# Optimization experiments

Measured on AMD Instinct MI355X. Metric: run time of the kernel, lower is better.

Reference implementation:

```python
import jax, jax.numpy as jnp
import numpy as np

C = 1024
H = 16
EPS = 1e-5

def layernorm(x, g, b):
    mu = jnp.mean(x, axis=-1, keepdims=True)
    var = jnp.var(x, axis=-1, keepdims=True)
    return (x - mu) * jax.lax.rsqrt(var + EPS) * g + b

def setup_inputs() -> dict:
    key = jax.random.key(0)
    ks = jax.random.split(key, 12)
    s = lambda fan: 1.0 / np.sqrt(fan)
    return {
        "x": jax.random.normal(ks[0], (2, 2048, C), jnp.float32),
        "W_qkv": jax.random.uniform(ks[1], (C, 3 * C), jnp.float32, -s(C), s(C)),
        "W_o": jax.random.uniform(ks[2], (C, C), jnp.float32, -s(C), s(C)),
        "b_o": jnp.zeros((C,), jnp.float32),
        "g1": jnp.ones((C,), jnp.float32),
        "beta1": jnp.zeros((C,), jnp.float32),
        "g2": jnp.ones((C,), jnp.float32),
        "beta2": jnp.zeros((C,), jnp.float32),
        "W_ff1": jax.random.uniform(ks[3], (C, 4 * C), jnp.float32, -s(C), s(C)),
        "b_ff1": jnp.zeros((4 * C,), jnp.float32),
        "W_ff2": jax.random.uniform(ks[4], (4 * C, C), jnp.float32, -s(4 * C), s(4 * C)),
        "b_ff2": jnp.zeros((C,), jnp.float32),
    }

def reference(x, W_qkv, W_o, b_o, g1, beta1, g2, beta2, W_ff1, b_ff1, W_ff2, b_ff2):
    B, T, _ = x.shape
    hd = C // H  # head dim
    # --- self-attention on norm1(x) ---
    h = layernorm(x, g1, beta1)
    qkv = h @ W_qkv                      # [B,T,3C]
    q, k, v = jnp.split(qkv, 3, axis=-1)
    reshp = lambda t: t.reshape(B, T, H, hd).transpose(0, 2, 1, 3)  # [B,H,T,hd]
    q, k, v = reshp(q), reshp(k), reshp(v)
    att = jnp.einsum("bhqd,bhkd->bhqk", q, k) * (hd ** -0.5)
    causal = jnp.tril(jnp.ones((T, T), bool))
    att = jnp.where(causal, att, -jnp.inf)
    att = jax.nn.softmax(att, axis=-1)
    out = jnp.einsum("bhqk,bhkd->bhqd", att, v)
    out = out.transpose(0, 2, 1, 3).reshape(B, T, C)
    x = x + out @ W_o + b_o
    # --- feed-forward on norm2(x) ---
    h = layernorm(x, g2, beta2)
    h = jax.nn.relu(h @ W_ff1 + b_ff1) @ W_ff2 + b_ff2
    return x + h
```

## Files before the change

### kernel.cpp

```cpp
#include <hip/hip_runtime.h>
#include <hip/hip_bf16.h>
#include <stdint.h>


typedef __attribute__((ext_vector_type(8))) short bf16x8;
typedef __attribute__((ext_vector_type(4))) float f32x4;

#define MFMA16(a, b, c) __builtin_amdgcn_mfma_f32_16x16x32_bf16((a), (b), (c), 0, 0, 0)

__device__ __forceinline__ void gload16(const void* g, void* l) {
    __builtin_amdgcn_global_load_lds(
        (const __attribute__((address_space(1))) char*)g,
        (__attribute__((address_space(3))) char*)l, 16, 0, 0);
}

__device__ __forceinline__ int xcd_swizzle(int flat, int nblk) {
    if ((nblk & 7) == 0) {
        const int per = nblk >> 3;
        flat = (flat & 7) * per + (flat >> 3);
    }
    return flat;
}

__global__ __launch_bounds__(256) void tconv_all(
    const float* __restrict__ w0, __hip_bfloat16* __restrict__ o0,
    const float* __restrict__ w1, __hip_bfloat16* __restrict__ o1,
    const float* __restrict__ w2, __hip_bfloat16* __restrict__ o2,
    const float* __restrict__ w3, __hip_bfloat16* __restrict__ o3) {
    __shared__ float tile[64][33];
    const int f = blockIdx.x;
    const float* in; __hip_bfloat16* out; int K, N, nx, t;
    if (f < 1536)      { in = w0; out = o0; K = 1024; N = 3072; nx = 96;  t = f; }
    else if (f < 2048) { in = w1; out = o1; K = 1024; N = 1024; nx = 32;  t = f - 1536; }
    else if (f < 4096) { in = w2; out = o2; K = 1024; N = 4096; nx = 128; t = f - 2048; }
    else               { in = w3; out = o3; K = 4096; N = 1024; nx = 32;  t = f - 4096; }
    const int n0 = (t % nx) * 32, k0 = (t / nx) * 64;
    const int tx = threadIdx.x, ty = threadIdx.y;
#pragma unroll
    for (int i = 0; i < 8; i++)
        tile[i * 8 + ty][tx] = in[(size_t)(k0 + i * 8 + ty) * N + n0 + tx];
    __syncthreads();
    for (int i = ty; i < 32; i += 8) {
        const unsigned short lo =
            __bfloat16_as_ushort(__float2bfloat16(tile[2 * tx][i]));
        const unsigned short hi =
            __bfloat16_as_ushort(__float2bfloat16(tile[2 * tx + 1][i]));
        *(uint32_t*)(out + (size_t)(n0 + i) * K + k0 + 2 * tx) =
            ((uint32_t)hi << 16) | lo;
    }
}

__global__ __launch_bounds__(256) void ln_k(const float* __restrict__ x,
                                            const float* __restrict__ g,
                                            const float* __restrict__ beta,
                                            __hip_bfloat16* __restrict__ out) {
    const int row = blockIdx.x;
    const int tid = threadIdx.x;
    float4 v = ((const float4*)(x + (size_t)row * 1024))[tid];
    float s  = v.x + v.y + v.z + v.w;
    float s2 = v.x * v.x + v.y * v.y + v.z * v.z + v.w * v.w;
    for (int off = 1; off < 64; off <<= 1) {
        s  += __shfl_xor(s,  off, 64);
        s2 += __shfl_xor(s2, off, 64);
    }
    __shared__ float ss[4], ss2[4];
    const int w = tid >> 6, lane = tid & 63;
    if (lane == 0) { ss[w] = s; ss2[w] = s2; }
    __syncthreads();
    s  = ss[0] + ss[1] + ss[2] + ss[3];
    s2 = ss2[0] + ss2[1] + ss2[2] + ss2[3];
    const float mu  = s * (1.0f / 1024.0f);
    const float var = s2 * (1.0f / 1024.0f) - mu * mu;
    const float rs  = rsqrtf(var + 1e-5f);
    float4 gv = ((const float4*)g)[tid];
    float4 bv = ((const float4*)beta)[tid];
    __hip_bfloat16* o = out + (size_t)row * 1024 + tid * 4;
    o[0] = __float2bfloat16((v.x - mu) * rs * gv.x + bv.x);
    o[1] = __float2bfloat16((v.y - mu) * rs * gv.y + bv.y);
    o[2] = __float2bfloat16((v.z - mu) * rs * gv.z + bv.z);
    o[3] = __float2bfloat16((v.w - mu) * rs * gv.w + bv.w);
}

template <int BIAS, int RELU>
__global__ __launch_bounds__(512, 2) void gemm256_k(const __hip_bfloat16* __restrict__ A,
                                                    const __hip_bfloat16* __restrict__ Bt,
                                                    const float* __restrict__ bias,
                                                    __hip_bfloat16* __restrict__ out,
                                                    int M, int N, int K) {
    __align__(16) __shared__ __hip_bfloat16 As[2][2][128 * 64];
    __align__(16) __shared__ __hip_bfloat16 Bs[2][2][128 * 64];

    const int tid  = threadIdx.x;
    const int lane = tid & 63, w = tid >> 6;
    const int wm = w >> 2, wn = w & 3;
    const int nbx = gridDim.x;
    const int flat = xcd_swizzle(blockIdx.y * nbx + blockIdx.x, nbx * gridDim.y);
    const int m0 = (flat / nbx) * 256, n0 = (flat % nbx) * 256;
    const int l16 = lane & 15, quad = lane >> 4;

    const int srw = lane >> 3;
    const int scn = ((lane & 7) - srw) & 7;

    const __hip_bfloat16* gA[2][2];
    const __hip_bfloat16* gB[2][2];
#pragma unroll
    for (int h = 0; h < 2; h++)
#pragma unroll
        for (int i = 0; i < 2; i++) {
            const int r = h * 128 + i * 64 + w * 8 + srw;
            gA[h][i] = A  + (size_t)(m0 + r) * K + scn * 8;
            gB[h][i] = Bt + (size_t)(n0 + r) * K + scn * 8;
        }

    int offA[2][4], offB[2][2];
#pragma unroll
    for (int s = 0; s < 2; s++) {
#pragma unroll
        for (int t = 0; t < 4; t++) {
            const int r = t * 16 + l16;
            offA[s][t] = (r * 8 + ((s * 4 + quad + (r & 7)) & 7)) * 16;
        }
#pragma unroll
        for (int t = 0; t < 2; t++) {
            const int r = (wn & 1) * 64 + t * 16 + l16;
            offB[s][t] = (r * 8 + ((s * 4 + quad + (r & 7)) & 7)) * 16;
        }
    }
    const char* AsW = (const char*)&As[0][wm][0];
    const char* BsW = (const char*)&Bs[0][wn >> 1][0];

    f32x4 acc[8][4] = {};
    bf16x8 a[2][4], b[2][2];

    const int NT = K >> 6;

#define STG_A(ST, SH, D)                                                      \
    do { if ((ST) < NT) {                                                     \
        _Pragma("unroll") for (int i = 0; i < 2; i++)                         \
            gload16(gA[SH][i] + (size_t)(ST) * 64,                            \
                    &As[D][SH][(i * 64 + w * 8) * 64]);                       \
    } } while (0)
#define STG_B(ST, SH, D)                                                      \
    do { if ((ST) < NT) {                                                     \
        _Pragma("unroll") for (int i = 0; i < 2; i++)                         \
            gload16(gB[SH][i] + (size_t)(ST) * 64,                            \
                    &Bs[D][SH][(i * 64 + w * 8) * 64]);                       \
    } } while (0)
#define VM_NONE do {} while (0)
#define VM_P(X)                                                               \
    do { if ((X) < NT) asm volatile("s_waitcnt vmcnt(2)" ::: "memory");       \
         else          asm volatile("s_waitcnt vmcnt(0)" ::: "memory");       \
    } while (0)

#define PH(RDA, MH, RDB, NH, D, STG, VM)                                      \
    do {                                                                      \
        if (RDA) {                                                            \
            _Pragma("unroll") for (int s = 0; s < 2; s++)                     \
            _Pragma("unroll") for (int t = 0; t < 4; t++)                     \
                a[s][t] = *(const bf16x8*)(AsW + (D) * 32768 + (MH) * 8192 +  \
                                           offA[s][t]);                       \
        }                                                                     \
        if (RDB) {                                                            \
            _Pragma("unroll") for (int s = 0; s < 2; s++)                     \
            _Pragma("unroll") for (int t = 0; t < 2; t++)                     \
                b[s][t] = *(const bf16x8*)(BsW + (D) * 32768 + (NH) * 4096 +  \
                                           offB[s][t]);                       \
        }                                                                     \
        STG;                                                                  \
        __builtin_amdgcn_s_barrier();                                         \
        asm volatile("" ::: "memory");                                        \
        __builtin_amdgcn_s_setprio(1);                                        \
        _Pragma("unroll") for (int s = 0; s < 2; s++)                         \
        _Pragma("unroll") for (int ti = 0; ti < 4; ti++)                      \
        _Pragma("unroll") for (int tj = 0; tj < 2; tj++)                      \
            acc[(MH) * 4 + ti][(NH) * 2 + tj] =                               \
                MFMA16(a[s][ti], b[s][tj], acc[(MH) * 4 + ti][(NH) * 2 + tj]);\
        __builtin_amdgcn_s_setprio(0);                                        \
        VM;                                                                   \
        __builtin_amdgcn_s_barrier();                                         \
        asm volatile("" ::: "memory");                                        \
    } while (0)

    STG_A(0, 0, 0); STG_A(0, 1, 0); STG_B(0, 0, 0); STG_B(0, 1, 0);
    STG_A(1, 0, 1);
    asm volatile("s_waitcnt vmcnt(2)" ::: "memory");
    __builtin_amdgcn_s_barrier();
    asm volatile("" ::: "memory");

    for (int T = 0; T < NT; T += 2) {
        PH(1, 0, 1, 0, 0, STG_A(T + 1, 1, 1), VM_NONE);
        PH(0, 0, 1, 1, 0, STG_B(T + 1, 0, 1), VM_NONE);
        PH(1, 1, 0, 1, 0, STG_B(T + 1, 1, 1), VM_NONE);
        PH(0, 1, 1, 0, 0, STG_A(T + 2, 0, 0), VM_P(T + 2));
        PH(1, 0, 1, 0, 1, STG_A(T + 2, 1, 0), VM_NONE);
        PH(0, 0, 1, 1, 1, STG_B(T + 2, 0, 0), VM_NONE);
        PH(1, 1, 0, 1, 1, STG_B(T + 2, 1, 0), VM_NONE);
        PH(0, 1, 1, 0, 1, STG_A(T + 3, 0, 1), VM_P(T + 3));
    }
#undef PH
#undef VM_P
#undef VM_NONE
#undef STG_B
#undef STG_A

#pragma unroll
    for (int mt = 0; mt < 8; mt++)
#pragma unroll
        for (int nt = 0; nt < 4; nt++) {
            const int row = m0 + wm * 128 + mt * 16 + quad * 4;
            const int col = n0 + wn * 64 + nt * 16 + l16;
            const float bv = BIAS ? bias[col] : 0.0f;
#pragma unroll
            for (int r = 0; r < 4; r++) {
                float v = acc[mt][nt][r] + bv;
                if (RELU) v = v > 0.0f ? v : 0.0f;
                out[(size_t)(row + r) * N + col] = __float2bfloat16(v);
            }
        }
}

template <int BIAS, int RELU, int RESID, int OUTBF>
__global__ __launch_bounds__(256, 4) void gemm6464_k(const __hip_bfloat16* __restrict__ A,
                                                     const __hip_bfloat16* __restrict__ Bt,
                                                     const float* __restrict__ bias,
                                                     const float* __restrict__ resid,
                                                     void* __restrict__ out,
                                                     int M, int N, int K) {
    __align__(16) __shared__ __hip_bfloat16 As[2][64 * 64];
    __align__(16) __shared__ __hip_bfloat16 Bs[2][64 * 64];

    const int tid  = threadIdx.x;
    const int lane = tid & 63, w = tid >> 6;
    const int wm = w >> 1, wn = w & 1;
    const int nbx = gridDim.x;
    const int flat = xcd_swizzle(blockIdx.y * nbx + blockIdx.x, nbx * gridDim.y);
    const int m0 = (flat / nbx) * 64, n0 = (flat % nbx) * 64;
    const int l16 = lane & 15, quad = lane >> 4;

    const int srw = lane >> 3;
    const int scn = ((lane & 7) - srw) & 7;

    const __hip_bfloat16* ga[2];
    const __hip_bfloat16* gb[2];
#pragma unroll
    for (int i = 0; i < 2; i++) {
        const int row = i * 32 + w * 8 + srw;
        ga[i] = A  + (size_t)(m0 + row) * K + scn * 8;
        gb[i] = Bt + (size_t)(n0 + row) * K + scn * 8;
    }

    int offA[2][2], offB[2][2];
#pragma unroll
    for (int s = 0; s < 2; s++)
#pragma unroll
        for (int t = 0; t < 2; t++) {
            const int rA = wm * 32 + t * 16 + l16;
            offA[s][t] = (rA * 8 + ((s * 4 + quad + (rA & 7)) & 7)) * 16;
            const int rB = wn * 32 + t * 16 + l16;
            offB[s][t] = (rB * 8 + ((s * 4 + quad + (rB & 7)) & 7)) * 16;
        }

    f32x4 acc[2][2] = {};

#pragma unroll
    for (int i = 0; i < 2; i++) {
        gload16(ga[i], As[0] + (i * 256 + w * 64) * 8);
        gload16(gb[i], Bs[0] + (i * 256 + w * 64) * 8);
        ga[i] += 64; gb[i] += 64;
    }

    const int niter = K >> 6;
    for (int it = 0; it < niter; it++) {
        const int buf = it & 1;
        __syncthreads();
        if (it + 1 < niter) {
#pragma unroll
            for (int i = 0; i < 2; i++) {
                gload16(ga[i], As[buf ^ 1] + (i * 256 + w * 64) * 8);
                gload16(gb[i], Bs[buf ^ 1] + (i * 256 + w * 64) * 8);
                ga[i] += 64; gb[i] += 64;
            }
        }

#pragma unroll
        for (int s = 0; s < 2; s++) {
            bf16x8 af[2], bfr[2];
#pragma unroll
            for (int t = 0; t < 2; t++) {
                af[t]  = *(const bf16x8*)((const char*)As[buf] + offA[s][t]);
                bfr[t] = *(const bf16x8*)((const char*)Bs[buf] + offB[s][t]);
            }
#pragma unroll
            for (int mt = 0; mt < 2; mt++)
#pragma unroll
                for (int nt = 0; nt < 2; nt++)
                    acc[mt][nt] = MFMA16(af[mt], bfr[nt], acc[mt][nt]);
        }
    }

#pragma unroll
    for (int mt = 0; mt < 2; mt++)
#pragma unroll
        for (int nt = 0; nt < 2; nt++) {
            const int row = m0 + wm * 32 + mt * 16 + quad * 4;
            const int col = n0 + wn * 32 + nt * 16 + l16;
            const float bv = BIAS ? bias[col] : 0.0f;
#pragma unroll
            for (int r = 0; r < 4; r++) {
                float v = acc[mt][nt][r] + bv;
                if (RELU) v = v > 0.0f ? v : 0.0f;
                const size_t idx = (size_t)(row + r) * N + col;
                if (RESID) v += resid[idx];
                if (OUTBF) ((__hip_bfloat16*)out)[idx] = __float2bfloat16(v);
                else       ((float*)out)[idx] = v;
            }
        }
}

__global__ __launch_bounds__(256) void vtrans_k(const __hip_bfloat16* __restrict__ qkv,
                                                __hip_bfloat16* __restrict__ vt) {
    const int T = 2048, C3 = 3072;
    const int bh = blockIdx.y, b = bh >> 4, h = bh & 15;
    const int t0 = blockIdx.x * 64;
    const int tx = threadIdx.x, ty = threadIdx.y;
    __shared__ __hip_bfloat16 tile[64][65];
#pragma unroll
    for (int j = 0; j < 16; j++) {
        const int tl = ty * 16 + j;
        tile[tl][tx] = qkv[(size_t)(b * T + t0 + tl) * C3 + 2048 + h * 64 + tx];
    }
    __syncthreads();
#pragma unroll
    for (int j = 0; j < 16; j++) {
        const int d = ty * 16 + j;
        vt[((size_t)bh * 64 + d) * 2048 + t0 + tx] = tile[tx][d];
    }
}

__global__ __launch_bounds__(256, 3) void attn_k(const __hip_bfloat16* __restrict__ qkv,
                                                 const __hip_bfloat16* __restrict__ vt,
                                                 __hip_bfloat16* __restrict__ outp) {
    const int T = 2048, C3 = 3072;
    const int bh = blockIdx.x, b = bh >> 4, h = bh & 15;
    const int qt = 31 - blockIdx.y;
    const int q0 = qt * 64;
    const int tid = threadIdx.x, lane = tid & 63, w = tid >> 6;
    const int l16 = lane & 15, quad = lane >> 4;

    __align__(16) __shared__ __hip_bfloat16 Ks[2][64 * 64];
    __align__(16) __shared__ __hip_bfloat16 Vs[2][64 * 64];
    __align__(16) __shared__ __hip_bfloat16 Pw[4][16 * 72];

    const float sc = 0.125f * 1.44269504f;
    bf16x8 qf0, qf1;
    {
        const __hip_bfloat16* qp =
            qkv + (size_t)(b * T + q0 + w * 16 + l16) * C3 + h * 64;
        bf16x8 a = *(const bf16x8*)(qp + quad * 8);
        bf16x8 c = *(const bf16x8*)(qp + 32 + quad * 8);
#pragma unroll
        for (int i = 0; i < 8; i++) {
            union { unsigned int u; float f; } ua, uc;
            ua.u = ((unsigned int)(unsigned short)a[i]) << 16;
            uc.u = ((unsigned int)(unsigned short)c[i]) << 16;
            qf0[i] = (short)(__bfloat16_as_ushort(__float2bfloat16(ua.f * sc)));
            qf1[i] = (short)(__bfloat16_as_ushort(__float2bfloat16(uc.f * sc)));
        }
    }

    const int srw = lane >> 3;
    const int scn = ((lane & 7) - srw) & 7;
    const __hip_bfloat16* kp[2];
    const __hip_bfloat16* vp[2];
#pragma unroll
    for (int i = 0; i < 2; i++) {
        const int row = i * 32 + w * 8 + srw;
        kp[i] = qkv + (size_t)(b * T + row) * C3 + 1024 + h * 64 + scn * 8;
        vp[i] = vt + ((size_t)bh * 64 + row) * 2048 + scn * 8;
    }

    int offK[2][4];
#pragma unroll
    for (int s = 0; s < 2; s++)
#pragma unroll
        for (int t = 0; t < 4; t++) {
            const int rr = t * 16 + l16;
            offK[s][t] = (rr * 8 + ((s * 4 + quad + (rr & 7)) & 7)) * 16;
        }

    f32x4 oacc[4] = {};
    float lpart[4] = {0.0f, 0.0f, 0.0f, 0.0f};

#pragma unroll
    for (int i = 0; i < 2; i++) {
        gload16(kp[i], Ks[0] + (i * 256 + w * 64) * 8);
        gload16(vp[i], Vs[0] + (i * 256 + w * 64) * 8);
    }

    for (int kt = 0; kt <= qt; kt++) {
        const int buf = kt & 1;
        __syncthreads();
        if (kt < qt) {
#pragma unroll
            for (int i = 0; i < 2; i++) {
                gload16(kp[i] + (size_t)(kt + 1) * 64 * C3,
                        Ks[buf ^ 1] + (i * 256 + w * 64) * 8);
                gload16(vp[i] + (kt + 1) * 64,
                        Vs[buf ^ 1] + (i * 256 + w * 64) * 8);
            }
        }

        f32x4 s4[4];
#pragma unroll
        for (int nt = 0; nt < 4; nt++) {
            bf16x8 kf0 = *(const bf16x8*)((const char*)Ks[buf] + offK[0][nt]);
            bf16x8 kf1 = *(const bf16x8*)((const char*)Ks[buf] + offK[1][nt]);
            f32x4 z = {};
            z = MFMA16(qf0, kf0, z);
            z = MFMA16(qf1, kf1, z);
            s4[nt] = z;
        }

        const bool diag = (kt == qt);
        const int myrow = w * 16 + quad * 4;
#pragma unroll
        for (int nt = 0; nt < 4; nt++) {
            const int col = nt * 16 + l16;
#pragma unroll
            for (int r = 0; r < 4; r++) {
                float p = exp2f(s4[nt][r]);
                if (diag && col > myrow + r) p = 0.0f;
                lpart[r] += p;
                Pw[w][(quad * 4 + r) * 72 + col] = __float2bfloat16(p);
            }
        }

        asm volatile("s_waitcnt lgkmcnt(0)" ::: "memory");

        bf16x8 pf0 = *(const bf16x8*)(&Pw[w][l16 * 72 + quad * 8]);
        bf16x8 pf1 = *(const bf16x8*)(&Pw[w][l16 * 72 + 32 + quad * 8]);
#pragma unroll
        for (int dt = 0; dt < 4; dt++) {
            bf16x8 vf0 = *(const bf16x8*)((const char*)Vs[buf] + offK[0][dt]);
            bf16x8 vf1 = *(const bf16x8*)((const char*)Vs[buf] + offK[1][dt]);
            oacc[dt] = MFMA16(pf0, vf0, oacc[dt]);
            oacc[dt] = MFMA16(pf1, vf1, oacc[dt]);
        }
    }

#pragma unroll
    for (int off = 1; off < 16; off <<= 1)
#pragma unroll
        for (int r = 0; r < 4; r++)
            lpart[r] += __shfl_xor(lpart[r], off, 64);

    float rl[4];
#pragma unroll
    for (int r = 0; r < 4; r++) rl[r] = 1.0f / lpart[r];
#pragma unroll
    for (int dt = 0; dt < 4; dt++)
#pragma unroll
        for (int r = 0; r < 4; r++) {
            const int row = q0 + w * 16 + quad * 4 + r;
            outp[(size_t)(b * T + row) * 1024 + h * 64 + dt * 16 + l16] =
                __float2bfloat16(oacc[dt][r] * rl[r]);
        }
}

extern "C" void kernel_launch(void* const* d_in, const int* in_sizes, int n_in,
                              void* d_out, int out_size, void* d_ws, size_t ws_size,
                              hipStream_t stream) {
    const float* x     = (const float*)d_in[0];
    const float* Wqkv  = (const float*)d_in[1];
    const float* Wo    = (const float*)d_in[2];
    const float* b_o   = (const float*)d_in[3];
    const float* g1    = (const float*)d_in[4];
    const float* beta1 = (const float*)d_in[5];
    const float* g2    = (const float*)d_in[6];
    const float* beta2 = (const float*)d_in[7];
    const float* Wff1  = (const float*)d_in[8];
    const float* bff1  = (const float*)d_in[9];
    const float* Wff2  = (const float*)d_in[10];
    const float* bff2  = (const float*)d_in[11];

    char* ws = (char*)d_ws;
    size_t off = 0;
    auto alloc = [&](size_t bytes) {
        void* p = ws + off;
        off += (bytes + 255) & ~(size_t)255;
        return p;
    };
    __hip_bfloat16* Wqkv_t = (__hip_bfloat16*)alloc(3072ULL * 1024 * 2);
    __hip_bfloat16* Wo_t   = (__hip_bfloat16*)alloc(1024ULL * 1024 * 2);
    __hip_bfloat16* Wff1_t = (__hip_bfloat16*)alloc(4096ULL * 1024 * 2);
    __hip_bfloat16* Wff2_t = (__hip_bfloat16*)alloc(1024ULL * 4096 * 2);
    __hip_bfloat16* h_bf   = (__hip_bfloat16*)alloc(4096ULL * 1024 * 2);
    __hip_bfloat16* qkv_bf = (__hip_bfloat16*)alloc(4096ULL * 3072 * 2);
    __hip_bfloat16* att_bf = (__hip_bfloat16*)alloc(4096ULL * 1024 * 2);
    float*          x2     = (float*)alloc(4096ULL * 1024 * 4);
    __hip_bfloat16* ff1_bf = qkv_bf;
    __hip_bfloat16* vt     = (__hip_bfloat16*)x2;

    tconv_all<<<6144, dim3(32, 8), 0, stream>>>(Wqkv, Wqkv_t, Wo, Wo_t,
                                                Wff1, Wff1_t, Wff2, Wff2_t);

    ln_k<<<4096, 256, 0, stream>>>(x, g1, beta1, h_bf);
    gemm256_k<0, 0><<<dim3(3072 / 256, 4096 / 256), 512, 0, stream>>>(
        h_bf, Wqkv_t, nullptr, qkv_bf, 4096, 3072, 1024);
    vtrans_k<<<dim3(32, 32), dim3(64, 4), 0, stream>>>(qkv_bf, vt);
    attn_k<<<dim3(32, 32), 256, 0, stream>>>(qkv_bf, vt, att_bf);
    gemm6464_k<1, 0, 1, 0><<<dim3(1024 / 64, 4096 / 64), 256, 0, stream>>>(
        att_bf, Wo_t, b_o, x, x2, 4096, 1024, 1024);
    ln_k<<<4096, 256, 0, stream>>>(x2, g2, beta2, h_bf);
    gemm256_k<1, 1><<<dim3(4096 / 256, 4096 / 256), 512, 0, stream>>>(
        h_bf, Wff1_t, bff1, ff1_bf, 4096, 4096, 1024);
    gemm6464_k<1, 0, 1, 0><<<dim3(1024 / 64, 4096 / 64), 256, 0, stream>>>(
        ff1_bf, Wff2_t, bff2, x2, (float*)d_out, 4096, 1024, 4096);
}
```

Baseline: 307.8 us.

## Replace 64x64 output GEMM with 128x128 four-stage pipelined kernel and MFMA priority

Swaps the 64x64-tile GEMM used for the attention output projection and FF2 for a 128x128-tile, 512-thread kernel. It uses a 4-buffer LDS ring with split A/B staging, explicit vmcnt waits and barriers, and raised wave priority around MFMA bursts. The attention kernel also raises priority around its two MFMA loops. This aims for more data reuse per tile and better overlap of global loads with compute. The cost is fewer blocks (256) for these N=1024 GEMMs, which may underfill the CUs, plus 128KB of LDS per block.

Result: no change. 308.8 us (+0.3%).

```diff
diff --git a/kernel.cpp b/kernel.cpp
--- a/kernel.cpp
+++ b/kernel.cpp
@@ -220,89 +220,129 @@
 }
 
 template <int BIAS, int RELU, int RESID, int OUTBF>
-__global__ __launch_bounds__(256, 4) void gemm6464_k(const __hip_bfloat16* __restrict__ A,
+__global__ __launch_bounds__(512, 2) void gemm128p_k(const __hip_bfloat16* __restrict__ A,
                                                      const __hip_bfloat16* __restrict__ Bt,
                                                      const float* __restrict__ bias,
                                                      const float* __restrict__ resid,
                                                      void* __restrict__ out,
                                                      int M, int N, int K) {
-    __align__(16) __shared__ __hip_bfloat16 As[2][64 * 64];
-    __align__(16) __shared__ __hip_bfloat16 Bs[2][64 * 64];
+    __align__(16) __shared__ __hip_bfloat16 As[4][128 * 64];
+    __align__(16) __shared__ __hip_bfloat16 Bs[4][128 * 64];
 
     const int tid  = threadIdx.x;
     const int lane = tid & 63, w = tid >> 6;
-    const int wm = w >> 1, wn = w & 1;
+    const int wm = w >> 2, wn = w & 3;
     const int nbx = gridDim.x;
     const int flat = xcd_swizzle(blockIdx.y * nbx + blockIdx.x, nbx * gridDim.y);
-    const int m0 = (flat / nbx) * 64, n0 = (flat % nbx) * 64;
+    const int m0 = (flat / nbx) * 128, n0 = (flat % nbx) * 128;
     const int l16 = lane & 15, quad = lane >> 4;
 
     const int srw = lane >> 3;
     const int scn = ((lane & 7) - srw) & 7;
 
-    const __hip_bfloat16* ga[2];
-    const __hip_bfloat16* gb[2];
-#pragma unroll
-    for (int i = 0; i < 2; i++) {
-        const int row = i * 32 + w * 8 + srw;
-        ga[i] = A  + (size_t)(m0 + row) * K + scn * 8;
-        gb[i] = Bt + (size_t)(n0 + row) * K + scn * 8;
-    }
-
-    int offA[2][2], offB[2][2];
-#pragma unroll
-    for (int s = 0; s < 2; s++)
+    const __hip_bfloat16* gA[2];
+    const __hip_bfloat16* gB[2];
+#pragma unroll
+    for (int h = 0; h < 2; h++) {
+        const int r = h * 64 + w * 8 + srw;
+        gA[h] = A  + (size_t)(m0 + r) * K + scn * 8;
+        gB[h] = Bt + (size_t)(n0 + r) * K + scn * 8;
+    }
+
+    int offA[2][4], offB[2][2];
+#pragma unroll
+    for (int s = 0; s < 2; s++) {
+#pragma unroll
+        for (int t = 0; t < 4; t++) {
+            const int r = wm * 64 + t * 16 + l16;
+            offA[s][t] = (r * 8 + ((s * 4 + quad + (r & 7)) & 7)) * 16;
+        }
 #pragma unroll
         for (int t = 0; t < 2; t++) {
-            const int rA = wm * 32 + t * 16 + l16;
-            offA[s][t] = (rA * 8 + ((s * 4 + quad + (rA & 7)) & 7)) * 16;
-            const int rB = wn * 32 + t * 16 + l16;
-            offB[s][t] = (rB * 8 + ((s * 4 + quad + (rB & 7)) & 7)) * 16;
-        }
-
-    f32x4 acc[2][2] = {};
-
-#pragma unroll
-    for (int i = 0; i < 2; i++) {
-        gload16(ga[i], As[0] + (i * 256 + w * 64) * 8);
-        gload16(gb[i], Bs[0] + (i * 256 + w * 64) * 8);
-        ga[i] += 64; gb[i] += 64;
-    }
-
-    const int niter = K >> 6;
-    for (int it = 0; it < niter; it++) {
-        const int buf = it & 1;
-        __syncthreads();
-        if (it + 1 < niter) {
-#pragma unroll
-            for (int i = 0; i < 2; i++) {
-                gload16(ga[i], As[buf ^ 1] + (i * 256 + w * 64) * 8);
-                gload16(gb[i], Bs[buf ^ 1] + (i * 256 + w * 64) * 8);
-                ga[i] += 64; gb[i] += 64;
-            }
-        }
-
-#pragma unroll
-        for (int s = 0; s < 2; s++) {
-            bf16x8 af[2], bfr[2];
-#pragma unroll
-            for (int t = 0; t < 2; t++) {
-                af[t]  = *(const bf16x8*)((const char*)As[buf] + offA[s][t]);
-                bfr[t] = *(const bf16x8*)((const char*)Bs[buf] + offB[s][t]);
-            }
-#pragma unroll
-            for (int mt = 0; mt < 2; mt++)
-#pragma unroll
-                for (int nt = 0; nt < 2; nt++)
-                    acc[mt][nt] = MFMA16(af[mt], bfr[nt], acc[mt][nt]);
-        }
-    }
-
-#pragma unroll
-    for (int mt = 0; mt < 2; mt++)
+            const int r = wn * 32 + t * 16 + l16;
+            offB[s][t] = (r * 8 + ((s * 4 + quad + (r & 7)) & 7)) * 16;
+        }
+    }
+
+    f32x4 acc[4][2] = {};
+    bf16x8 b[2][2];
+
+    const int NT = K >> 6;
+
+#define STGA(T, BUF)                                                          \
+    do { if ((T) < NT) {                                                      \
+        _Pragma("unroll") for (int h = 0; h < 2; h++)                         \
+            gload16(gA[h] + (size_t)(T) * 64,                                 \
+                    &As[BUF][(h * 64 + w * 8) * 64]);                         \
+    } } while (0)
+#define STGB(T, BUF)                                                          \
+    do { if ((T) < NT) {                                                      \
+        _Pragma("unroll") for (int h = 0; h < 2; h++)                         \
+            gload16(gB[h] + (size_t)(T) * 64,                                 \
+                    &Bs[BUF][(h * 64 + w * 8) * 64]);                         \
+    } } while (0)
+#define VM0 do {} while (0)
+#define VMC(X)                                                                \
+    do { if ((X) < NT) asm volatile("s_waitcnt vmcnt(4)" ::: "memory");       \
+         else          asm volatile("s_waitcnt vmcnt(0)" ::: "memory");       \
+    } while (0)
+
+#define PH128(CB, MH, RDB, STG, VM)                                           \
+    do {                                                                      \
+        bf16x8 a2[2][2];                                                      \
+        _Pragma("unroll") for (int s = 0; s < 2; s++)                         \
+        _Pragma("unroll") for (int j = 0; j < 2; j++)                         \
+            a2[s][j] = *(const bf16x8*)((const char*)As[CB] +                 \
+                                        offA[s][(MH) * 2 + j]);               \
+        if (RDB) {                                                            \
+            _Pragma("unroll") for (int s = 0; s < 2; s++)                     \
+            _Pragma("unroll") for (int j = 0; j < 2; j++)                     \
+                b[s][j] = *(const bf16x8*)((const char*)Bs[CB] + offB[s][j]); \
+        }                                                                     \
+        STG;                                                                  \
+        __builtin_amdgcn_s_barrier();                                         \
+        asm volatile("" ::: "memory");                                        \
+        __builtin_amdgcn_s_setprio(1);                                        \
+        _Pragma("unroll") for (int s = 0; s < 2; s++)                         \
+        _Pragma("unroll") for (int mt = 0; mt < 2; mt++)                      \
+        _Pragma("unroll") for (int nt = 0; nt < 2; nt++)                      \
+            acc[(MH) * 2 + mt][nt] =                                          \
+                MFMA16(a2[s][mt], b[s][nt], acc[(MH) * 2 + mt][nt]);          \
+        __builtin_amdgcn_s_setprio(0);                                        \
+        VM;                                                                   \
+        __builtin_amdgcn_s_barrier();                                         \
+        asm volatile("" ::: "memory");                                        \
+    } while (0)
+
+#define PAIR(T, C0, C1, S0, S1)                                               \
+    do {                                                                      \
+        PH128(C0, 0, 1, STGA(T + 2, S0), VM0);                                \
+        PH128(C0, 1, 0, STGB(T + 2, S0), VMC(T + 2));                         \
+        PH128(C1, 0, 1, STGA(T + 3, S1), VM0);                                \
+        PH128(C1, 1, 0, STGB(T + 3, S1), VMC(T + 3));                         \
+    } while (0)
+
+    STGA(0, 0); STGB(0, 0); STGA(1, 1); STGB(1, 1);
+    asm volatile("s_waitcnt vmcnt(4)" ::: "memory");
+    __builtin_amdgcn_s_barrier();
+    asm volatile("" ::: "memory");
+
+    for (int T = 0; T < NT; T += 4) {
+        PAIR(T, 0, 1, 2, 3);
+        PAIR(T + 2, 2, 3, 0, 1);
+    }
+#undef PAIR
+#undef PH128
+#undef VMC
+#undef VM0
+#undef STGB
+#undef STGA
+
+#pragma unroll
+    for (int mt = 0; mt < 4; mt++)
 #pragma unroll
         for (int nt = 0; nt < 2; nt++) {
-            const int row = m0 + wm * 32 + mt * 16 + quad * 4;
+            const int row = m0 + wm * 64 + mt * 16 + quad * 4;
             const int col = n0 + wn * 32 + nt * 16 + l16;
             const float bv = BIAS ? bias[col] : 0.0f;
 #pragma unroll
@@ -411,6 +451,7 @@
         }
 
         f32x4 s4[4];
+        __builtin_amdgcn_s_setprio(1);
 #pragma unroll
         for (int nt = 0; nt < 4; nt++) {
             bf16x8 kf0 = *(const bf16x8*)((const char*)Ks[buf] + offK[0][nt]);
@@ -420,6 +461,7 @@
             z = MFMA16(qf1, kf1, z);
             s4[nt] = z;
         }
+        __builtin_amdgcn_s_setprio(0);
 
         const bool diag = (kt == qt);
         const int myrow = w * 16 + quad * 4;
@@ -439,6 +481,7 @@
 
         bf16x8 pf0 = *(const bf16x8*)(&Pw[w][l16 * 72 + quad * 8]);
         bf16x8 pf1 = *(const bf16x8*)(&Pw[w][l16 * 72 + 32 + quad * 8]);
+        __builtin_amdgcn_s_setprio(1);
 #pragma unroll
         for (int dt = 0; dt < 4; dt++) {
             bf16x8 vf0 = *(const bf16x8*)((const char*)Vs[buf] + offK[0][dt]);
@@ -446,6 +489,7 @@
             oacc[dt] = MFMA16(pf0, vf0, oacc[dt]);
             oacc[dt] = MFMA16(pf1, vf1, oacc[dt]);
         }
+        __builtin_amdgcn_s_setprio(0);
     }
 
 #pragma unroll
@@ -509,11 +553,11 @@
         h_bf, Wqkv_t, nullptr, qkv_bf, 4096, 3072, 1024);
     vtrans_k<<<dim3(32, 32), dim3(64, 4), 0, stream>>>(qkv_bf, vt);
     attn_k<<<dim3(32, 32), 256, 0, stream>>>(qkv_bf, vt, att_bf);
-    gemm6464_k<1, 0, 1, 0><<<dim3(1024 / 64, 4096 / 64), 256, 0, stream>>>(
+    gemm128p_k<1, 0, 1, 0><<<dim3(1024 / 128, 4096 / 128), 512, 0, stream>>>(
         att_bf, Wo_t, b_o, x, x2, 4096, 1024, 1024);
     ln_k<<<4096, 256, 0, stream>>>(x2, g2, beta2, h_bf);
     gemm256_k<1, 1><<<dim3(4096 / 256, 4096 / 256), 512, 0, stream>>>(
         h_bf, Wff1_t, bff1, ff1_bf, 4096, 4096, 1024);
-    gemm6464_k<1, 0, 1, 0><<<dim3(1024 / 64, 4096 / 64), 256, 0, stream>>>(
+    gemm128p_k<1, 0, 1, 0><<<dim3(1024 / 128, 4096 / 128), 512, 0, stream>>>(
         ff1_bf, Wff2_t, bff2, x2, (float*)d_out, 4096, 1024, 4096);
 }
```

## Split-K the FF2 GEMM on the 256x256 kernel and raise MFMA priority in attention

Applied to the files above, without the earlier changes.

The FF2 projection (K=4096) moves from the 64x64 tile kernel to the 256x256 tile kernel with a 4-way split-K. Each split writes fp32 partial sums, and a new reduce kernel adds the partials, bias and residual. The attention kernel also wraps its MFMA sections in s_setprio(1) so those waves get higher scheduling priority. The aim is better data reuse from the larger tiles, at the cost of 64 MB of partial-sum writes and reads plus one extra launch.

New measurement: 322.9 us. 4.9% more time.

```diff
diff --git a/kernel.cpp b/kernel.cpp
--- a/kernel.cpp
+++ b/kernel.cpp
@@ -81,12 +81,12 @@
     o[3] = __float2bfloat16((v.w - mu) * rs * gv.w + bv.w);
 }
 
-template <int BIAS, int RELU>
+template <int BIAS, int RELU, int PART>
 __global__ __launch_bounds__(512, 2) void gemm256_k(const __hip_bfloat16* __restrict__ A,
                                                     const __hip_bfloat16* __restrict__ Bt,
                                                     const float* __restrict__ bias,
-                                                    __hip_bfloat16* __restrict__ out,
-                                                    int M, int N, int K) {
+                                                    void* __restrict__ out,
+                                                    int M, int N, int K, int kper) {
     __align__(16) __shared__ __hip_bfloat16 As[2][2][128 * 64];
     __align__(16) __shared__ __hip_bfloat16 Bs[2][2][128 * 64];
 
@@ -96,6 +96,7 @@
     const int nbx = gridDim.x;
     const int flat = xcd_swizzle(blockIdx.y * nbx + blockIdx.x, nbx * gridDim.y);
     const int m0 = (flat / nbx) * 256, n0 = (flat % nbx) * 256;
+    const int z  = blockIdx.z;
     const int l16 = lane & 15, quad = lane >> 4;
 
     const int srw = lane >> 3;
@@ -108,8 +109,8 @@
 #pragma unroll
         for (int i = 0; i < 2; i++) {
             const int r = h * 128 + i * 64 + w * 8 + srw;
-            gA[h][i] = A  + (size_t)(m0 + r) * K + scn * 8;
-            gB[h][i] = Bt + (size_t)(n0 + r) * K + scn * 8;
+            gA[h][i] = A  + (size_t)(m0 + r) * K + (size_t)z * kper + scn * 8;
+            gB[h][i] = Bt + (size_t)(n0 + r) * K + (size_t)z * kper + scn * 8;
         }
 
     int offA[2][4], offB[2][2];
@@ -132,7 +133,7 @@
     f32x4 acc[8][4] = {};
     bf16x8 a[2][4], b[2][2];
 
-    const int NT = K >> 6;
+    const int NT = kper >> 6;
 
 #define STG_A(ST, SH, D)                                                      \
     do { if ((ST) < NT) {                                                     \
@@ -209,14 +210,36 @@
         for (int nt = 0; nt < 4; nt++) {
             const int row = m0 + wm * 128 + mt * 16 + quad * 4;
             const int col = n0 + wn * 64 + nt * 16 + l16;
-            const float bv = BIAS ? bias[col] : 0.0f;
+            const float bv = (BIAS && !PART) ? bias[col] : 0.0f;
 #pragma unroll
             for (int r = 0; r < 4; r++) {
                 float v = acc[mt][nt][r] + bv;
                 if (RELU) v = v > 0.0f ? v : 0.0f;
-                out[(size_t)(row + r) * N + col] = __float2bfloat16(v);
+                const size_t idx = (size_t)(row + r) * N + col;
+                if (PART) ((float*)out)[(size_t)z * M * N + idx] = v;
+                else ((__hip_bfloat16*)out)[idx] = __float2bfloat16(v);
             }
         }
+}
+
+__global__ __launch_bounds__(256) void reduce4_k(const float* __restrict__ parts,
+                                                 const float* __restrict__ bias,
+                                                 const float* __restrict__ resid,
+                                                 float* __restrict__ out) {
+    const size_t f = (size_t)blockIdx.x * 256 + threadIdx.x;
+    const size_t STRIDE = 4096ULL * 1024 / 4;
+    float4 a = ((const float4*)parts)[f];
+    float4 b = ((const float4*)parts)[f + STRIDE];
+    float4 c = ((const float4*)parts)[f + 2 * STRIDE];
+    float4 d = ((const float4*)parts)[f + 3 * STRIDE];
+    float4 rv = ((const float4*)resid)[f];
+    float4 bv = ((const float4*)bias)[f & 255];
+    float4 o;
+    o.x = a.x + b.x + c.x + d.x + rv.x + bv.x;
+    o.y = a.y + b.y + c.y + d.y + rv.y + bv.y;
+    o.z = a.z + b.z + c.z + d.z + rv.z + bv.z;
+    o.w = a.w + b.w + c.w + d.w + rv.w + bv.w;
+    ((float4*)out)[f] = o;
 }
 
 template <int BIAS, int RELU, int RESID, int OUTBF>
@@ -411,6 +434,7 @@
         }
 
         f32x4 s4[4];
+        __builtin_amdgcn_s_setprio(1);
 #pragma unroll
         for (int nt = 0; nt < 4; nt++) {
             bf16x8 kf0 = *(const bf16x8*)((const char*)Ks[buf] + offK[0][nt]);
@@ -420,6 +444,7 @@
             z = MFMA16(qf1, kf1, z);
             s4[nt] = z;
         }
+        __builtin_amdgcn_s_setprio(0);
 
         const bool diag = (kt == qt);
         const int myrow = w * 16 + quad * 4;
@@ -439,6 +464,7 @@
 
         bf16x8 pf0 = *(const bf16x8*)(&Pw[w][l16 * 72 + quad * 8]);
         bf16x8 pf1 = *(const bf16x8*)(&Pw[w][l16 * 72 + 32 + quad * 8]);
+        __builtin_amdgcn_s_setprio(1);
 #pragma unroll
         for (int dt = 0; dt < 4; dt++) {
             bf16x8 vf0 = *(const bf16x8*)((const char*)Vs[buf] + offK[0][dt]);
@@ -446,6 +472,7 @@
             oacc[dt] = MFMA16(pf0, vf0, oacc[dt]);
             oacc[dt] = MFMA16(pf1, vf1, oacc[dt]);
         }
+        __builtin_amdgcn_s_setprio(0);
     }
 
 #pragma unroll
@@ -498,6 +525,7 @@
     __hip_bfloat16* qkv_bf = (__hip_bfloat16*)alloc(4096ULL * 3072 * 2);
     __hip_bfloat16* att_bf = (__hip_bfloat16*)alloc(4096ULL * 1024 * 2);
     float*          x2     = (float*)alloc(4096ULL * 1024 * 4);
+    float*          parts  = (float*)alloc(4ULL * 4096 * 1024 * 4);
     __hip_bfloat16* ff1_bf = qkv_bf;
     __hip_bfloat16* vt     = (__hip_bfloat16*)x2;
 
@@ -505,15 +533,16 @@
                                                 Wff1, Wff1_t, Wff2, Wff2_t);
 
     ln_k<<<4096, 256, 0, stream>>>(x, g1, beta1, h_bf);
-    gemm256_k<0, 0><<<dim3(3072 / 256, 4096 / 256), 512, 0, stream>>>(
-        h_bf, Wqkv_t, nullptr, qkv_bf, 4096, 3072, 1024);
+    gemm256_k<0, 0, 0><<<dim3(3072 / 256, 4096 / 256, 1), 512, 0, stream>>>(
+        h_bf, Wqkv_t, nullptr, qkv_bf, 4096, 3072, 1024, 1024);
     vtrans_k<<<dim3(32, 32), dim3(64, 4), 0, stream>>>(qkv_bf, vt);
     attn_k<<<dim3(32, 32), 256, 0, stream>>>(qkv_bf, vt, att_bf);
     gemm6464_k<1, 0, 1, 0><<<dim3(1024 / 64, 4096 / 64), 256, 0, stream>>>(
         att_bf, Wo_t, b_o, x, x2, 4096, 1024, 1024);
     ln_k<<<4096, 256, 0, stream>>>(x2, g2, beta2, h_bf);
-    gemm256_k<1, 1><<<dim3(4096 / 256, 4096 / 256), 512, 0, stream>>>(
-        h_bf, Wff1_t, bff1, ff1_bf, 4096, 4096, 1024);
-    gemm6464_k<1, 0, 1, 0><<<dim3(1024 / 64, 4096 / 64), 256, 0, stream>>>(
-        ff1_bf, Wff2_t, bff2, x2, (float*)d_out, 4096, 1024, 4096);
-}
+    gemm256_k<1, 1, 0><<<dim3(4096 / 256, 4096 / 256, 1), 512, 0, stream>>>(
+        h_bf, Wff1_t, bff1, ff1_bf, 4096, 4096, 1024, 1024);
+    gemm256_k<0, 0, 1><<<dim3(1024 / 256, 4096 / 256, 4), 512, 0, stream>>>(
+        ff1_bf, Wff2_t, nullptr, parts, 4096, 1024, 4096, 1024);
+    reduce4_k<<<4096, 256, 0, stream>>>(parts, bff2, x2, (float*)d_out);
+}
```
